# Optimization experiments

Hardware: AMD Instinct MI355X
Metric: run time of the kernel (lower is better)

Reference implementation:

```python
import jax, jax.numpy as jnp
import numpy as np

B, N, C, T = 16, 96, 4, 256
H, DT, DP, P, TOUT = 128, 16, 128, 4, 64
DIN = H + DT
LEAK = 0.1


def setup_inputs():
    key = jax.random.key(0)
    ks = jax.random.split(key, 16)
    rn = lambda k, shp, s: jax.random.normal(k, shp, dtype=jnp.float32) * s
    return {
        'X_in': jax.random.normal(ks[0], (B, N, C, T), dtype=jnp.float32),
        'phases': jax.random.randint(ks[1], (B,), 0, P),
        'gru_Wih': rn(ks[2], (N, 3 * H, C), 0.1),
        'gru_Whh': rn(ks[3], (N, 3 * H, H), 0.08),
        'gru_bih': jnp.zeros((N, 3 * H), jnp.float32),
        'gru_bhh': jnp.zeros((N, 3 * H), jnp.float32),
        'ln_g': jnp.ones((H,), jnp.float32),
        'ln_b': jnp.zeros((H,), jnp.float32),
        'tpos_w': rn(ks[4], (DT, 1), 0.5),
        'tpos_b': jnp.zeros((DT,), jnp.float32),
        'S': rn(ks[5], (P, N, N), 0.1),
        'G': rn(ks[6], (P, N), 0.1),
        'W_self': rn(ks[7], (DP, DIN), 0.05),
        'W_neigh': rn(ks[8], (DP, DIN), 0.05),
        'sn_u': jax.random.normal(ks[9], (DP,), dtype=jnp.float32),
        'k_w': rn(ks[10], (DP, DP), 0.05),
        'v_w': rn(ks[11], (DP, DP), 0.05),
        'cell_Wih': rn(ks[12], (3 * DP, DP + C), 0.05),
        'cell_Whh': rn(ks[13], (3 * DP, DP), 0.05),
        'cell_bih': jnp.zeros((3 * DP,), jnp.float32),
        'cell_bhh': jnp.zeros((3 * DP,), jnp.float32),
        'read_w': rn(ks[14], (C, DP), 0.05),
        'read_b': jnp.zeros((C,), jnp.float32),
        'log_tau': jnp.asarray(np.log(1.0 / np.sqrt(DP)), dtype=jnp.float32),
    }


def _encode(X, Wih, Whh, bih, bhh, g, b):
    # Per-region GRU (distinct weights per node), torch gate order r,z,n.
    xs = jnp.moveaxis(X, -1, 0)  # [T,B,N,C]
    h0 = jnp.zeros((B, N, H), X.dtype)
    def step(h, xt):
        gi = jnp.einsum('bnc,ngc->bng', xt, Wih) + bih
        gh = jnp.einsum('bnh,ngh->bng', h, Whh) + bhh
        ir, iz, inn = jnp.split(gi, 3, axis=-1)
        hr, hz, hn = jnp.split(gh, 3, axis=-1)
        r = jax.nn.sigmoid(ir + hr)
        z = jax.nn.sigmoid(iz + hz)
        n = jnp.tanh(inn + r * hn)
        hnew = (1.0 - z) * n + z * h
        return hnew, hnew
    _, ys = jax.lax.scan(step, h0, xs)  # [T,B,N,H]
    mu = ys.mean(-1, keepdims=True)
    var = ys.var(-1, keepdims=True)
    ys = (ys - mu) * jax.lax.rsqrt(var + 1e-5) * g + b
    return jnp.moveaxis(ys, 0, 2)  # [B,N,T,H]


def _phase_adj(S, G, phases):
    I = jnp.eye(N, dtype=S.dtype)
    S0 = S * (1.0 - I)
    denom = jnp.clip(jnp.abs(S0).sum(-1, keepdims=True), 1e-6, None)
    An = S0 / denom
    gg = jax.nn.softplus(G) + 1e-6
    gg = gg * (N / jnp.clip(gg.sum(-1, keepdims=True), 1e-6, None))
    return An[phases] * gg[phases][..., None]  # [B,N,N]


def _spectral_normalize(W, u):
    v = W.T @ u
    v = v / (jnp.linalg.norm(v) + 1e-12)
    u2 = W @ v
    u2 = u2 / (jnp.linalg.norm(u2) + 1e-12)
    u2 = jax.lax.stop_gradient(u2)
    v = jax.lax.stop_gradient(v)
    sigma = u2 @ (W @ v)
    return W / sigma


def _head(Z, A, k_w, v_w, cWih, cWhh, cbih, cbhh, rw, rb, log_tau):
    BN = B * N
    M = Z.reshape(BN, T, DP)
    K = M @ k_w.T
    V = M @ v_w.T
    h0 = M[:, -1, :]
    y0 = jnp.zeros((BN, C), Z.dtype)
    scale = jnp.exp(log_tau)
    def step(carry, _):
        h, y = carry
        yb = y.reshape(B, N, C)
        yb = yb + 0.3 * jnp.einsum('bij,bjc->bic', A, yb)
        y = yb.reshape(BN, C)
        scores = jnp.einsum('mtd,md->mt', K, h) * scale
        alpha = jax.nn.softmax(scores, axis=-1)
        ctx = jnp.einsum('mt,mtd->md', alpha, V)
        inp = jnp.concatenate([ctx, y], axis=-1)
        gi = inp @ cWih.T + cbih
        gh = h @ cWhh.T + cbhh
        ir, iz, inn = jnp.split(gi, 3, axis=-1)
        hr, hz, hn = jnp.split(gh, 3, axis=-1)
        r = jax.nn.sigmoid(ir + hr)
        z = jax.nn.sigmoid(iz + hz)
        n = jnp.tanh(inn + r * hn)
        h = (1.0 - z) * n + z * h
        y_t = h @ rw.T + rb + y
        return (h, y_t), y_t
    _, ys = jax.lax.scan(step, (h0, y0), None, length=TOUT)  # [TOUT,BN,C]
    return jnp.transpose(ys, (1, 2, 0)).reshape(B, N, C, TOUT)


def _forward(X_in, phases, gru_Wih, gru_Whh, gru_bih, gru_bhh, ln_g, ln_b,
             tpos_w, tpos_b, S, G, W_self, W_neigh, sn_u, k_w, v_w,
             cell_Wih, cell_Whh, cell_bih, cell_bhh, read_w, read_b, log_tau):
    Henc = _encode(X_in, gru_Wih, gru_Whh, gru_bih, gru_bhh, ln_g, ln_b)  # [B,N,T,H]
    t = jnp.linspace(0.0, 1.0, T).astype(jnp.float32).reshape(T, 1)
    u = jnp.tanh(t @ tpos_w.T + tpos_b)  # [T,DT]
    u = jnp.broadcast_to(u[None, None], (B, N, T, DT))
    Hc = jnp.concatenate([Henc, u], axis=-1)  # [B,N,T,DIN]
    A = _phase_adj(S, G, phases)
    Wsn = _spectral_normalize(W_neigh, sn_u)
    Hs = Hc @ W_self.T
    Hn = Hc @ Wsn.T
    Zn = jnp.einsum('bij,bjtd->bitd', A, Hn)
    Zpre = Hs + Zn
    Z = jnp.where(Zpre >= 0, Zpre, LEAK * Zpre)
    Y_delta = _head(Z, A, k_w, v_w, cell_Wih, cell_Whh, cell_bih, cell_bhh,
                    read_w, read_b, log_tau)
    x_last = X_in[..., -1]  # [B,N,C]
    Y_hat = x_last[..., None] + Y_delta
    return Y_hat, Y_hat[..., 0:1]


def reference(X_in, phases, gru_Wih, gru_Whh, gru_bih, gru_bhh, ln_g, ln_b,
              tpos_w, tpos_b, S, G, W_self, W_neigh, sn_u, k_w, v_w,
              cell_Wih, cell_Whh, cell_bih, cell_bhh, read_w, read_b, log_tau):
    return _forward(X_in, phases, gru_Wih, gru_Whh, gru_bih, gru_bhh, ln_g, ln_b,
                    tpos_w, tpos_b, S, G, W_self, W_neigh, sn_u, k_w, v_w,
                    cell_Wih, cell_Whh, cell_bih, cell_bhh, read_w, read_b, log_tau)
```

## Files before the change

kernel.cpp:

```cpp
#include <hip/hip_runtime.h>
#include <stdint.h>

typedef unsigned int u32;
typedef unsigned short u16;
typedef __attribute__((ext_vector_type(8))) short s8v;
typedef __attribute__((ext_vector_type(8))) __bf16 bf16x8;
typedef __attribute__((ext_vector_type(4))) float f32x4;

#define OFF_HENC 0ull
#define OFF_M    100663296ull
#define OFF_APF  201326592ull
#define OFF_APB  201474048ull
#define OFF_WNF  201547776ull
#define OFF_WSF  201588736ull
#define OFF_KWF  201629696ull
#define OFF_VWF  201662464ull
#define OFF_WIHF 201695232ull
#define OFF_WHHF 201793536ull
#define OFF_CWY  201891840ull
#define OFF_UPAD 201897984ull
#define OFF_SCAL 201914368ull
#define OFF_HH   201914624ull
#define OFF_Y    202701056ull

__device__ __forceinline__ u16 f2bf(float f) {
  u32 u = __float_as_uint(f);
  u32 r = u + 0x7fffu + ((u >> 16) & 1u);
  return (u16)(r >> 16);
}
__device__ __forceinline__ float bf2f(u16 h) { return __uint_as_float(((u32)h) << 16); }
__device__ __forceinline__ float blo(u32 u) { return __uint_as_float(u << 16); }
__device__ __forceinline__ float bhi(u32 u) { return __uint_as_float(u & 0xffff0000u); }
__device__ __forceinline__ float sigm(float x) { return 1.f / (1.f + __expf(-x)); }
__device__ __forceinline__ float tanh_f(float x) {
  float a = fminf(fabsf(x), 15.f);
  float e = __expf(2.f * a);
  float t = (e - 1.f) / (e + 1.f);
  return copysignf(t, x);
}
__device__ __forceinline__ f32x4 MFMA(s8v a, s8v b, f32x4 c) {
  return __builtin_amdgcn_mfma_f32_16x16x32_bf16(
      __builtin_bit_cast(bf16x8, a), __builtin_bit_cast(bf16x8, b), c, 0, 0, 0);
}

__global__ void k0a(const float* __restrict__ S, const float* __restrict__ G,
                    const float* __restrict__ Wn, const float* __restrict__ snu,
                    const float* __restrict__ logtau, const float* __restrict__ tpw,
                    const float* __restrict__ tpb, const float* __restrict__ cWih,
                    float* __restrict__ Apf, u16* __restrict__ Apb,
                    float* __restrict__ scal, u16* __restrict__ upad,
                    float* __restrict__ cWy) {
  int tid = threadIdx.x;
  int blk = blockIdx.x;
  if (blk < 4) {
    int p = blk;
    __shared__ float gg[96];
    __shared__ float gfac;
    if (tid < 96) {
      float x = G[p * 96 + tid];
      float sp = fmaxf(x, 0.f) + log1pf(__expf(-fabsf(x)));
      gg[tid] = sp + 1e-6f;
    }
    __syncthreads();
    if (tid == 0) {
      float s = 0;
      for (int i = 0; i < 96; ++i) s += gg[i];
      gfac = 96.f / fmaxf(s, 1e-6f);
    }
    __syncthreads();
    if (tid < 96) {
      int i = tid;
      const float* srow = S + ((size_t)p * 96 + i) * 96;
      float den = 0;
      for (int j = 0; j < 96; ++j) { float v = (j == i) ? 0.f : srow[j]; den += fabsf(v); }
      den = fmaxf(den, 1e-6f);
      float sc = gg[i] * gfac / den;
      for (int j = 0; j < 96; ++j) {
        float v = (j == i) ? 0.f : srow[j];
        float a = v * sc;
        Apf[((size_t)p * 96 + i) * 96 + j] = a;
        Apb[((size_t)p * 96 + i) * 96 + j] = f2bf(a);
      }
    }
  } else if (blk == 4) {
    __shared__ float sv[144];
    __shared__ float su[128];
    __shared__ float snorm;
    if (tid < 144) {
      float a = 0;
      for (int d = 0; d < 128; ++d) a += Wn[d * 144 + tid] * snu[d];
      sv[tid] = a;
    }
    __syncthreads();
    if (tid == 0) {
      float s = 0;
      for (int j = 0; j < 144; ++j) s += sv[j] * sv[j];
      snorm = sqrtf(s) + 1e-12f;
    }
    __syncthreads();
    if (tid < 144) sv[tid] = sv[tid] / snorm;
    __syncthreads();
    if (tid < 128) {
      float a = 0;
      for (int j = 0; j < 144; ++j) a += Wn[tid * 144 + j] * sv[j];
      su[tid] = a;
    }
    __syncthreads();
    if (tid == 0) {
      float ss = 0;
      for (int d = 0; d < 128; ++d) ss += su[d] * su[d];
      float nu = sqrtf(ss);
      float sigma = ss / (nu + 1e-12f);
      scal[0] = 1.f / sigma;
      scal[1] = __expf(logtau[0]);
    }
  } else {
    for (int idx = tid; idx < 256 * 32; idx += 256) {
      int t = idx >> 5, kk = idx & 31;
      float v = 0.f;
      if (kk < 16) v = tanh_f((float)t * (1.f / 255.f) * tpw[kk] + tpb[kk]);
      upad[idx] = f2bf(v);
    }
    for (int idx = tid; idx < 1536; idx += 256)
      cWy[idx] = cWih[(idx >> 2) * 132 + 128 + (idx & 3)];
  }
}
// ... 144 lines not shown
  const int b = blockIdx.x >> 8, t = blockIdx.x & 255;
  const int p = phases[b];
  const int lane = threadIdx.x & 63, w = threadIdx.x >> 6;
  const int colt = lane & 15, grp = lane >> 4;
  __shared__ __align__(16) u16 Hc[96][168];
  __shared__ __align__(16) u16 HnT[128][104];
  __shared__ float lnG[128], lnB[128];

  const u16* src = Henc + ((size_t)b * 96 * 256 + t) * 128;
  for (int u = threadIdx.x; u < 96 * 16; u += 256) {
    int j = u >> 4, ch = u & 15;
    *(uint4*)&Hc[j][ch * 8] = *(const uint4*)(src + (size_t)j * 256 * 128 + ch * 8);
  }
  for (int u = threadIdx.x; u < 96 * 16; u += 256) {
    int j = u >> 4, ch = u & 15;
    *(u32*)&Hc[j][128 + ch * 2] = *(const u32*)(upad + t * 32 + ch * 2);
  }
  if (threadIdx.x < 128) {
    lnG[threadIdx.x] = lng[threadIdx.x];
    lnB[threadIdx.x] = lnb[threadIdx.x];
  }
  __syncthreads();
  if (threadIdx.x < 96) {
    int j = threadIdx.x;
    float s = 0.f, q = 0.f;
#pragma unroll 4
    for (int d = 0; d < 128; ++d) {
      float v = bf2f(Hc[j][d]);
      s += v; q += v * v;
    }
    float mu = s * (1.f / 128.f);
    float var = q * (1.f / 128.f) - mu * mu;
    float rs = rsqrtf(var + 1e-5f);
#pragma unroll 4
    for (int d = 0; d < 128; ++d) {
      float v = bf2f(Hc[j][d]);
      Hc[j][d] = f2bf((v - mu) * rs * lnG[d] + lnB[d]);
    }
  }
  __syncthreads();
  for (int jj = 0; jj < 12; ++jj) {
    int job = w * 12 + jj;
    int jt = job >> 3, ct = job & 7;
    f32x4 acc = {0.f, 0.f, 0.f, 0.f};
#pragma unroll
    for (int kq = 0; kq < 5; ++kq) {
      s8v a = *(const s8v*)(const void*)&Hc[jt * 16 + colt][kq * 32 + grp * 8];
      acc = MFMA(a, WnF[(ct * 5 + kq) * 64 + lane], acc);
    }
    int d = ct * 16 + colt, j0 = jt * 16 + grp * 4;
    u32 w0 = ((u32)f2bf(acc[1]) << 16) | f2bf(acc[0]);
    u32 w1 = ((u32)f2bf(acc[3]) << 16) | f2bf(acc[2]);
    *(u32*)&HnT[d][j0] = w0;
    *(u32*)&HnT[d][j0 + 2] = w1;
  }
  __syncthreads();
  for (int jj = 0; jj < 12; ++jj) {
    int job = w * 12 + jj;
    int it = job >> 3, ct = job & 7;
    f32x4 accZ = {0.f, 0.f, 0.f, 0.f}, accS = accZ;
#pragma unroll
    for (int kq = 0; kq < 3; ++kq) {
      s8v a = *(const s8v*)(const void*)(Apb + ((size_t)p * 96 + it * 16 + colt) * 96 + kq * 32 + grp * 8);
      s8v bb = *(const s8v*)(const void*)&HnT[ct * 16 + colt][kq * 32 + grp * 8];
      accZ = MFMA(a, bb, accZ);
    }
#pragma unroll
    for (int kq = 0; kq < 5; ++kq) {
      s8v a = *(const s8v*)(const void*)&Hc[it * 16 + colt][kq * 32 + grp * 8];
      accS = MFMA(a, WsF[(ct * 5 + kq) * 64 + lane], accS);
    }
    int d = ct * 16 + colt;
#pragma unroll
    for (int r = 0; r < 4; ++r) {
      int i = it * 16 + grp * 4 + r;
      float z = accS[r] + accZ[r];
      z = z >= 0.f ? z : 0.1f * z;
      M[(((size_t)b * 96 + i) * 256 + t) * 128 + d] = f2bf(z);
      if (t == 255) hh[((size_t)b * 96 + i) * 128 + d] = z;
    }
  }
}

__launch_bounds__(512)
__global__ void k4_step(int k, const u16* __restrict__ M, float* __restrict__ hh,
                        const float* __restrict__ yin, float* __restrict__ yout,
                        const float* __restrict__ Apf, const int* __restrict__ phases,
                        const float* __restrict__ scal,
                        const s8v* __restrict__ kwF, const s8v* __restrict__ vwF,
                        const s8v* __restrict__ wiF, const s8v* __restrict__ whF,
                        const float* __restrict__ cWy, const float* __restrict__ cbih,
                        const float* __restrict__ cbhh, const float* __restrict__ rw,
                        const float* __restrict__ rb, const float* __restrict__ X,
                        float* __restrict__ out) {
  const int bl = blockIdx.x;
  const int b = bl >> 4, n0 = (bl & 15) * 6, m0 = b * 96 + n0;
  const int lane = threadIdx.x & 63, w = threadIdx.x >> 6;
  const int colt = lane & 15, grp = lane >> 4;
  __shared__ float hfl[6][128];
  __shared__ __align__(16) u16 hb[16][136];
  __shared__ __align__(16) u16 qb[6][128];
  __shared__ __align__(16) u16 sb[16][136];
  __shared__ __align__(16) u16 cxb[16][136];
  __shared__ __align__(16) float macc[6][16][128];
  __shared__ float mmd[6][16][2];
  __shared__ float gi_l[6][392];
  __shared__ float gh_l[6][392];
  __shared__ float ypl[6][4];
  const float scale = scal[1];

  for (int idx = threadIdx.x; idx < 2048; idx += 512) {
    int i = idx >> 7, d = idx & 127;
    float hv = 0.f;
    if (i < 6) {
      hv = hh[(size_t)(m0 + i) * 128 + d];
      hfl[i][d] = hv;
    } else {
      sb[i][d] = 0;
      cxb[i][d] = 0;
    }
    hb[i][d] = f2bf(hv);
  }
  if (w < 6) {
    int i = w, ni = n0 + w;
    const float* arow = Apf + ((size_t)phases[b] * 96 + ni) * 96;
    float acc[4] = {0.f, 0.f, 0.f, 0.f};
    for (int j = lane; j < 96; j += 64) {
      float av = arow[j];
      const float* yr = yin + ((size_t)b * 96 + j) * 4;
      acc[0] += av * yr[0]; acc[1] += av * yr[1];
      acc[2] += av * yr[2]; acc[3] += av * yr[3];
    }
#pragma unroll
    for (int mm = 1; mm < 64; mm <<= 1) {
#pragma unroll
      for (int c = 0; c < 4; ++c) acc[c] += __shfl_xor(acc[c], mm);
    }
    if (lane < 4) ypl[i][lane] = yin[((size_t)b * 96 + ni) * 4 + lane] + 0.3f * acc[lane];
  }
  __syncthreads();

  {
    int ct = w;
    f32x4 acc = {0.f, 0.f, 0.f, 0.f};
#pragma unroll
    for (int kq = 0; kq < 4; ++kq) {
      s8v a = *(const s8v*)(const void*)&hb[colt][kq * 32 + grp * 8];
      acc = MFMA(a, kwF[(ct * 4 + kq) * 64 + lane], acc);
    }
#pragma unroll
    for (int r = 0; r < 4; ++r) {
      int i = grp * 4 + r;
      if (i < 6) qb[i][ct * 16 + colt] = f2bf(acc[r] * scale);
    }
  }
  __syncthreads();

#pragma unroll 1
  for (int uu = 0; uu < 3; ++uu) {
    int u = w + uu * 8;
    int mi = u >> 2, qq = u & 3;
    float qf[8];
    const u32* qsrc = (const u32*)&qb[mi][colt * 8];
#pragma unroll
    for (int x = 0; x < 4; ++x) { u32 v = qsrc[x]; qf[2 * x] = blo(v); qf[2 * x + 1] = bhi(v); }
    const u16* mp = M + ((size_t)(m0 + mi) * 256 + qq * 64 + grp) * 128 + colt * 8;
    uint4 mv[16];
#pragma unroll
    for (int it = 0; it < 16; ++it) mv[it] = *(const uint4*)(mp + it * 512);
    float p[16];
#pragma unroll
    for (int it = 0; it < 16; ++it) {
      uint4 v = mv[it];
      float pp = blo(v.x) * qf[0] + bhi(v.x) * qf[1] + blo(v.y) * qf[2] + bhi(v.y) * qf[3]
               + blo(v.z) * qf[4] + bhi(v.z) * qf[5] + blo(v.w) * qf[6] + bhi(v.w) * qf[7];
      pp += __shfl_xor(pp, 1); pp += __shfl_xor(pp, 2);
      pp += __shfl_xor(pp, 4); pp += __shfl_xor(pp, 8);
      p[it] = pp;
    }
    float mx = p[0];
#pragma unroll
    for (int it = 1; it < 16; ++it) mx = fmaxf(mx, p[it]);
    float den = 0.f;
    float acc[8] = {0.f, 0.f, 0.f, 0.f, 0.f, 0.f, 0.f, 0.f};
#pragma unroll
    for (int it = 0; it < 16; ++it) {
      float wgt = __expf(p[it] - mx);
      den += wgt;
      uint4 v = mv[it];
      acc[0] += wgt * blo(v.x); acc[1] += wgt * bhi(v.x);
      acc[2] += wgt * blo(v.y); acc[3] += wgt * bhi(v.y);
      acc[4] += wgt * blo(v.z); acc[5] += wgt * bhi(v.z);
      acc[6] += wgt * blo(v.w); acc[7] += wgt * bhi(v.w);
    }
    int su = qq * 4 + grp;
    float* dst = &macc[mi][su][colt * 8];
#pragma unroll
    for (int j = 0; j < 8; ++j) dst[j] = acc[j];
    if (colt == 0) { mmd[mi][su][0] = mx; mmd[mi][su][1] = den; }
  }
  __syncthreads();

  if (w < 6) {
    int i = w;
    float MX = -3.0e38f;
#pragma unroll
    for (int uy = 0; uy < 16; ++uy) MX = fmaxf(MX, mmd[i][uy][0]);
    float DEN = 0.f, s0 = 0.f, s1 = 0.f;
    int c0 = lane * 2;
#pragma unroll
    for (int uy = 0; uy < 16; ++uy) {
      float fac = __expf(mmd[i][uy][0] - MX);
      DEN += fac * mmd[i][uy][1];
      s0 += fac * macc[i][uy][c0];
      s1 += fac * macc[i][uy][c0 + 1];
    }
    float rden = 1.f / DEN;
    *(u32*)&sb[i][c0] = ((u32)f2bf(s1 * rden) << 16) | f2bf(s0 * rden);
  }
  __syncthreads();

  {
    int ct = w;
    f32x4 acc = {0.f, 0.f, 0.f, 0.f};
#pragma unroll
    for (int kq = 0; kq < 4; ++kq) {
      s8v a = *(const s8v*)(const void*)&sb[colt][kq * 32 + grp * 8];
      acc = MFMA(a, vwF[(ct * 4 + kq) * 64 + lane], acc);
    }
#pragma unroll
    for (int r = 0; r < 4; ++r) {
      int i = grp * 4 + r;
      if (i < 6) cxb[i][ct * 16 + colt] = f2bf(acc[r]);
    }
  }
  __syncthreads();

  for (int jj = 0; jj < 6; ++jj) {
    int job = w * 6 + jj;
    int gsel = (job >= 24) ? 1 : 0;
    int ct = job - gsel * 24;
    const u16(*asrc)[136] = gsel ? hb : cxb;
    const s8v* wf = gsel ? whF : wiF;
    f32x4 acc = {0.f, 0.f, 0.f, 0.f};
#pragma unroll
    for (int kq = 0; kq < 4; ++kq) {
      s8v a = *(const s8v*)(const void*)&asrc[colt][kq * 32 + grp * 8];
      acc = MFMA(a, wf[(ct * 4 + kq) * 64 + lane], acc);
    }
    float* dst = gsel ? &gh_l[0][0] : &gi_l[0][0];
#pragma unroll
    for (int r = 0; r < 4; ++r) {
      int i = grp * 4 + r;
      if (i < 6) dst[i * 392 + ct * 16 + colt] = acc[r];
    }
  }
  __syncthreads();

  if (w < 6) {
    int i = w, m = m0 + i;
    float yp0 = ypl[i][0], yp1 = ypl[i][1], yp2 = ypl[i][2], yp3 = ypl[i][3];
    float hn2[2];
#pragma unroll
    for (int q = 0; q < 2; ++q) {
      int d = lane + q * 64;
      float gir = gi_l[i][d] + cbih[d];
      float giz = gi_l[i][d + 128] + cbih[d + 128];
      float gin = gi_l[i][d + 256] + cbih[d + 256];
      const float* wy0 = cWy + (size_t)d * 4;
      const float* wy1 = cWy + (size_t)(d + 128) * 4;
      const float* wy2 = cWy + (size_t)(d + 256) * 4;
      gir += yp0 * wy0[0] + yp1 * wy0[1] + yp2 * wy0[2] + yp3 * wy0[3];
      giz += yp0 * wy1[0] + yp1 * wy1[1] + yp2 * wy1[2] + yp3 * wy1[3];
      gin += yp0 * wy2[0] + yp1 * wy2[1] + yp2 * wy2[2] + yp3 * wy2[3];
      float ghr = gh_l[i][d] + cbhh[d];
      float ghz = gh_l[i][d + 128] + cbhh[d + 128];
      float ghn = gh_l[i][d + 256] + cbhh[d + 256];
      float rr = sigm(gir + ghr);
      float zz = sigm(giz + ghz);
      float nn = tanh_f(gin + rr * ghn);
      float hv = (1.f - zz) * nn + zz * hfl[i][d];
      hh[(size_t)m * 128 + d] = hv;
      hn2[q] = hv;
    }
    float p0 = hn2[0] * rw[0 * 128 + lane] + hn2[1] * rw[0 * 128 + lane + 64];
    float p1 = hn2[0] * rw[1 * 128 + lane] + hn2[1] * rw[1 * 128 + lane + 64];
    float p2 = hn2[0] * rw[2 * 128 + lane] + hn2[1] * rw[2 * 128 + lane + 64];
    float p3 = hn2[0] * rw[3 * 128 + lane] + hn2[1] * rw[3 * 128 + lane + 64];
#pragma unroll
    for (int mm = 1; mm < 64; mm <<= 1) {
      p0 += __shfl_xor(p0, mm); p1 += __shfl_xor(p1, mm);
      p2 += __shfl_xor(p2, mm); p3 += __shfl_xor(p3, mm);
    }
    if (lane < 4) {
      int c = lane;
      float pv = (c == 0) ? p0 : (c == 1) ? p1 : (c == 2) ? p2 : p3;
      float ypc = (c == 0) ? yp0 : (c == 1) ? yp1 : (c == 2) ? yp2 : yp3;
      float yv = pv + rb[c] + ypc;
      yout[(size_t)m * 4 + c] = yv;
      float xl = X[((size_t)m * 4 + c) * 256 + 255];
      float Yh = xl + yv;
      out[((size_t)m * 4 + c) * 64 + k] = Yh;
      if (k == 0) out[393216 + (size_t)m * 4 + c] = Yh;
    }
  }
}

extern "C" void kernel_launch(void* const* d_in, const int* in_sizes, int n_in,
                              void* d_out, int out_size, void* d_ws, size_t ws_size,
                              hipStream_t stream) {
  const float* X      = (const float*)d_in[0];
  const int*   phases = (const int*)d_in[1];
  const float* Wih    = (const float*)d_in[2];
  const float* Whh    = (const float*)d_in[3];
  const float* bih    = (const float*)d_in[4];
  const float* bhh    = (const float*)d_in[5];
  const float* lng    = (const float*)d_in[6];
  const float* lnb    = (const float*)d_in[7];
  const float* tpw    = (const float*)d_in[8];
  const float* tpb    = (const float*)d_in[9];
  const float* S      = (const float*)d_in[10];
  const float* G      = (const float*)d_in[11];
  const float* Wself  = (const float*)d_in[12];
  const float* Wneigh = (const float*)d_in[13];
  const float* snu    = (const float*)d_in[14];
  const float* kw     = (const float*)d_in[15];
  const float* vw     = (const float*)d_in[16];
  const float* cWih   = (const float*)d_in[17];
  const float* cWhh   = (const float*)d_in[18];
  const float* cbih   = (const float*)d_in[19];
  const float* cbhh   = (const float*)d_in[20];
  const float* rw     = (const float*)d_in[21];
  const float* rb     = (const float*)d_in[22];
  const float* ltau   = (const float*)d_in[23];

  char* ws = (char*)d_ws;
  u16*   Henc = (u16*)(ws + OFF_HENC);
  u16*   Mb   = (u16*)(ws + OFF_M);
  float* Apf  = (float*)(ws + OFF_APF);
  u16*   Apb  = (u16*)(ws + OFF_APB);
  u16*   WnF  = (u16*)(ws + OFF_WNF);
  u16*   WsF  = (u16*)(ws + OFF_WSF);
  u16*   kwF  = (u16*)(ws + OFF_KWF);
  u16*   vwF  = (u16*)(ws + OFF_VWF);
  u16*   wiF  = (u16*)(ws + OFF_WIHF);
  u16*   whF  = (u16*)(ws + OFF_WHHF);
  float* cWy  = (float*)(ws + OFF_CWY);
  u16*   upad = (u16*)(ws + OFF_UPAD);
  float* scal = (float*)(ws + OFF_SCAL);
  float* hh   = (float*)(ws + OFF_HH);

  hipMemsetAsync(ws + OFF_Y, 0, 49152, stream);
  hipLaunchKernelGGL(k0a, dim3(6), dim3(256), 0, stream,
                     S, G, Wneigh, snu, ltau, tpw, tpb, cWih, Apf, Apb, scal, upad, cWy);
  hipLaunchKernelGGL(k0b, dim3(672), dim3(256), 0, stream,
                     Wneigh, Wself, kw, vw, cWih, cWhh, scal, WnF, WsF, kwF, vwF, wiF, whF);
  hipLaunchKernelGGL(k1_encode, dim3(96), dim3(512), 0, stream,
                     X, Wih, Whh, bih, bhh, Henc);
  hipLaunchKernelGGL(k3_mix, dim3(4096), dim3(256), 0, stream,
                     Henc, upad, Apb, phases, lng, lnb,
                     (const s8v*)WnF, (const s8v*)WsF, Mb, hh);
  for (int k = 0; k < 64; ++k) {
    const float* yi = (const float*)(ws + OFF_Y + (size_t)(k & 1) * 24576);
    float*       yo = (float*)(ws + OFF_Y + (size_t)((k + 1) & 1) * 24576);
    hipLaunchKernelGGL(k4_step, dim3(256), dim3(512), 0, stream,
                       k, Mb, hh, yi, yo, Apf, phases, scal,
                       (const s8v*)kwF, (const s8v*)vwF, (const s8v*)wiF, (const s8v*)whF,
                       cWy, cbih, cbhh, rw, rb, X, (float*)d_out);
  }
}
```

Before: 2.158 ms.

## Fuse decode steps into persistent kernel with register-resident memory and group barriers

Replaces the 64 per-step launches of the decoder with one persistent kernel that loops over steps. Each block keeps its slice of the attention memory M in registers for all steps and carries the hidden state in shared memory. A per-batch atomic barrier synchronises the 16 blocks that share the y vector. It also uses bf16 dot2 for scores and stages small weights in LDS. The aim is to remove repeated global reads of M and launch overhead, at the cost of very high register pressure and a reliance on all blocks being co-resident.

Measured after the change: 7.835 ms. 263% more time.

```diff
diff --git a/kernel.cpp b/kernel.cpp
--- a/kernel.cpp
+++ b/kernel.cpp
@@ -5,6 +5,7 @@
 typedef unsigned short u16;
 typedef __attribute__((ext_vector_type(8))) short s8v;
 typedef __attribute__((ext_vector_type(8))) __bf16 bf16x8;
+typedef __attribute__((ext_vector_type(2))) __bf16 bf16x2;
 typedef __attribute__((ext_vector_type(4))) float f32x4;
 
 #define OFF_HENC 0ull
@@ -22,6 +23,7 @@
 #define OFF_SCAL 201914368ull
 #define OFF_HH   201914624ull
 #define OFF_Y    202701056ull
+#define OFF_BAR  202750208ull
 
 __device__ __forceinline__ u16 f2bf(float f) {
   u32 u = __float_as_uint(f);
@@ -42,6 +44,16 @@
   return __builtin_amdgcn_mfma_f32_16x16x32_bf16(
       __builtin_bit_cast(bf16x8, a), __builtin_bit_cast(bf16x8, b), c, 0, 0, 0);
 }
+
+#if __has_builtin(__builtin_amdgcn_fdot2_f32_bf16)
+#define HAS_DOT2 1
+__device__ __forceinline__ float dot2bf(u32 a, u32 b, float c) {
+  return __builtin_amdgcn_fdot2_f32_bf16(__builtin_bit_cast(bf16x2, a),
+                                         __builtin_bit_cast(bf16x2, b), c, false);
+}
+#else
+#define HAS_DOT2 0
+#endif
 
 __global__ void k0a(const float* __restrict__ S, const float* __restrict__ G,
                     const float* __restrict__ Wn, const float* __restrict__ snu,
@@ -352,34 +364,70 @@
   }
 }
 
-__launch_bounds__(512)
-__global__ void k4_step(int k, const u16* __restrict__ M, float* __restrict__ hh,
-                        const float* __restrict__ yin, float* __restrict__ yout,
-                        const float* __restrict__ Apf, const int* __restrict__ phases,
-                        const float* __restrict__ scal,
-                        const s8v* __restrict__ kwF, const s8v* __restrict__ vwF,
-                        const s8v* __restrict__ wiF, const s8v* __restrict__ whF,
-                        const float* __restrict__ cWy, const float* __restrict__ cbih,
-                        const float* __restrict__ cbhh, const float* __restrict__ rw,
-                        const float* __restrict__ rb, const float* __restrict__ X,
-                        float* __restrict__ out) {
+__device__ __forceinline__ void group_barrier(int* cnt, int* gen) {
+  __syncthreads();
+  if (threadIdx.x == 0) {
+    int g = __hip_atomic_load(gen, __ATOMIC_RELAXED, __HIP_MEMORY_SCOPE_AGENT);
+    int v = __hip_atomic_fetch_add(cnt, 1, __ATOMIC_ACQ_REL, __HIP_MEMORY_SCOPE_AGENT);
+    if (v == 15) {
+      __hip_atomic_store(cnt, 0, __ATOMIC_RELAXED, __HIP_MEMORY_SCOPE_AGENT);
+      __hip_atomic_fetch_add(gen, 1, __ATOMIC_ACQ_REL, __HIP_MEMORY_SCOPE_AGENT);
+    } else {
+      while (__hip_atomic_load(gen, __ATOMIC_ACQUIRE, __HIP_MEMORY_SCOPE_AGENT) == g)
+        __builtin_amdgcn_s_sleep(1);
+    }
+  }
+  __syncthreads();
+}
+
+__launch_bounds__(256, 1)
+__global__ void k4p(const u16* __restrict__ M, const float* __restrict__ hh,
+                    float* __restrict__ ybuf, int* __restrict__ bar,
+                    const float* __restrict__ Apf, const int* __restrict__ phases,
+                    const float* __restrict__ scal,
+                    const s8v* __restrict__ kwF, const s8v* __restrict__ vwF,
+                    const s8v* __restrict__ wiF, const s8v* __restrict__ whF,
+                    const float* __restrict__ cWy, const float* __restrict__ cbih,
+                    const float* __restrict__ cbhh, const float* __restrict__ rw,
+                    const float* __restrict__ rb, const float* __restrict__ X,
+                    float* __restrict__ out) {
   const int bl = blockIdx.x;
   const int b = bl >> 4, n0 = (bl & 15) * 6, m0 = b * 96 + n0;
   const int lane = threadIdx.x & 63, w = threadIdx.x >> 6;
   const int colt = lane & 15, grp = lane >> 4;
+  int* cnt = bar + b;
+  int* gen = bar + 16 + b;
+
   __shared__ float hfl[6][128];
   __shared__ __align__(16) u16 hb[16][136];
   __shared__ __align__(16) u16 qb[6][128];
   __shared__ __align__(16) u16 sb[16][136];
   __shared__ __align__(16) u16 cxb[16][136];
-  __shared__ __align__(16) float macc[6][16][128];
-  __shared__ float mmd[6][16][2];
+  __shared__ __align__(16) float macc[6][4][128];
+  __shared__ float mmd[6][4][2];
   __shared__ float gi_l[6][392];
   __shared__ float gh_l[6][392];
   __shared__ float ypl[6][4];
+  __shared__ float Arows[6][96];
+  __shared__ float cbl_i[384], cbl_h[384];
+  __shared__ float cWyl[384][4];
+  __shared__ float rwl[4][128];
+  __shared__ float rbl[4];
+  __shared__ float xlast[6][4];
+
+  const int p = phases[b];
   const float scale = scal[1];
 
-  for (int idx = threadIdx.x; idx < 2048; idx += 512) {
+  uint4 Mreg[6][16];
+#pragma unroll
+  for (int mi = 0; mi < 6; ++mi) {
+    const u16* base = M + (((size_t)(m0 + mi) * 256) + w * 64 + grp) * 128 + colt * 8;
+#pragma unroll
+    for (int it = 0; it < 16; ++it)
+      Mreg[mi][it] = *(const uint4*)(base + (size_t)it * 512);
+  }
+
+  for (int idx = threadIdx.x; idx < 2048; idx += 256) {
     int i = idx >> 7, d = idx & 127;
     float hv = 0.f;
     if (i < 6) {
@@ -391,188 +439,249 @@
     }
     hb[i][d] = f2bf(hv);
   }
-  if (w < 6) {
-    int i = w, ni = n0 + w;
-    const float* arow = Apf + ((size_t)phases[b] * 96 + ni) * 96;
-    float acc[4] = {0.f, 0.f, 0.f, 0.f};
-    for (int j = lane; j < 96; j += 64) {
-      float av = arow[j];
-      const float* yr = yin + ((size_t)b * 96 + j) * 4;
-      acc[0] += av * yr[0]; acc[1] += av * yr[1];
-      acc[2] += av * yr[2]; acc[3] += av * yr[3];
-    }
-#pragma unroll
-    for (int mm = 1; mm < 64; mm <<= 1) {
-#pragma unroll
-      for (int c = 0; c < 4; ++c) acc[c] += __shfl_xor(acc[c], mm);
-    }
-    if (lane < 4) ypl[i][lane] = yin[((size_t)b * 96 + ni) * 4 + lane] + 0.3f * acc[lane];
-  }
+  for (int idx = threadIdx.x; idx < 576; idx += 256) {
+    int i = idx / 96, j = idx % 96;
+    Arows[i][j] = Apf[((size_t)p * 96 + (n0 + i)) * 96 + j];
+  }
+  for (int idx = threadIdx.x; idx < 384; idx += 256) {
+    cbl_i[idx] = cbih[idx];
+    cbl_h[idx] = cbhh[idx];
+  }
+  for (int idx = threadIdx.x; idx < 1536; idx += 256)
+    (&cWyl[0][0])[idx] = cWy[idx];
+  for (int idx = threadIdx.x; idx < 512; idx += 256)
+    (&rwl[0][0])[idx] = rw[idx];
+  if (threadIdx.x < 4) rbl[threadIdx.x] = rb[threadIdx.x];
+  if (threadIdx.x < 24)
+    xlast[threadIdx.x >> 2][threadIdx.x & 3] =
+        X[((size_t)(m0 + (threadIdx.x >> 2)) * 4 + (threadIdx.x & 3)) * 256 + 255];
   __syncthreads();
 
-  {
-    int ct = w;
-    f32x4 acc = {0.f, 0.f, 0.f, 0.f};
-#pragma unroll
-    for (int kq = 0; kq < 4; ++kq) {
-      s8v a = *(const s8v*)(const void*)&hb[colt][kq * 32 + grp * 8];
-      acc = MFMA(a, kwF[(ct * 4 + kq) * 64 + lane], acc);
-    }
-#pragma unroll
-    for (int r = 0; r < 4; ++r) {
-      int i = grp * 4 + r;
-      if (i < 6) qb[i][ct * 16 + colt] = f2bf(acc[r] * scale);
-    }
-  }
-  __syncthreads();
-
 #pragma unroll 1
-  for (int uu = 0; uu < 3; ++uu) {
-    int u = w + uu * 8;
-    int mi = u >> 2, qq = u & 3;
-    float qf[8];
-    const u32* qsrc = (const u32*)&qb[mi][colt * 8];
-#pragma unroll
-    for (int x = 0; x < 4; ++x) { u32 v = qsrc[x]; qf[2 * x] = blo(v); qf[2 * x + 1] = bhi(v); }
-    const u16* mp = M + ((size_t)(m0 + mi) * 256 + qq * 64 + grp) * 128 + colt * 8;
-    uint4 mv[16];
-#pragma unroll
-    for (int it = 0; it < 16; ++it) mv[it] = *(const uint4*)(mp + it * 512);
-    float p[16];
-#pragma unroll
-    for (int it = 0; it < 16; ++it) {
-      uint4 v = mv[it];
-      float pp = blo(v.x) * qf[0] + bhi(v.x) * qf[1] + blo(v.y) * qf[2] + bhi(v.y) * qf[3]
-               + blo(v.z) * qf[4] + bhi(v.z) * qf[5] + blo(v.w) * qf[6] + bhi(v.w) * qf[7];
-      pp += __shfl_xor(pp, 1); pp += __shfl_xor(pp, 2);
-      pp += __shfl_xor(pp, 4); pp += __shfl_xor(pp, 8);
-      p[it] = pp;
-    }
-    float mx = p[0];
-#pragma unroll
-    for (int it = 1; it < 16; ++it) mx = fmaxf(mx, p[it]);
-    float den = 0.f;
-    float acc[8] = {0.f, 0.f, 0.f, 0.f, 0.f, 0.f, 0.f, 0.f};
-#pragma unroll
-    for (int it = 0; it < 16; ++it) {
-      float wgt = __expf(p[it] - mx);
-      den += wgt;
-      uint4 v = mv[it];
-      acc[0] += wgt * blo(v.x); acc[1] += wgt * bhi(v.x);
-      acc[2] += wgt * blo(v.y); acc[3] += wgt * bhi(v.y);
-      acc[4] += wgt * blo(v.z); acc[5] += wgt * bhi(v.z);
-      acc[6] += wgt * blo(v.w); acc[7] += wgt * bhi(v.w);
-    }
-    int su = qq * 4 + grp;
-    float* dst = &macc[mi][su][colt * 8];
-#pragma unroll
-    for (int j = 0; j < 8; ++j) dst[j] = acc[j];
-    if (colt == 0) { mmd[mi][su][0] = mx; mmd[mi][su][1] = den; }
-  }
-  __syncthreads();
-
-  if (w < 6) {
-    int i = w;
-    float MX = -3.0e38f;
-#pragma unroll
-    for (int uy = 0; uy < 16; ++uy) MX = fmaxf(MX, mmd[i][uy][0]);
-    float DEN = 0.f, s0 = 0.f, s1 = 0.f;
-    int c0 = lane * 2;
-#pragma unroll
-    for (int uy = 0; uy < 16; ++uy) {
-      float fac = __expf(mmd[i][uy][0] - MX);
-      DEN += fac * mmd[i][uy][1];
-      s0 += fac * macc[i][uy][c0];
-      s1 += fac * macc[i][uy][c0 + 1];
-    }
-    float rden = 1.f / DEN;
-    *(u32*)&sb[i][c0] = ((u32)f2bf(s1 * rden) << 16) | f2bf(s0 * rden);
-  }
-  __syncthreads();
-
-  {
-    int ct = w;
-    f32x4 acc = {0.f, 0.f, 0.f, 0.f};
-#pragma unroll
-    for (int kq = 0; kq < 4; ++kq) {
-      s8v a = *(const s8v*)(const void*)&sb[colt][kq * 32 + grp * 8];
-      acc = MFMA(a, vwF[(ct * 4 + kq) * 64 + lane], acc);
-    }
-#pragma unroll
-    for (int r = 0; r < 4; ++r) {
-      int i = grp * 4 + r;
-      if (i < 6) cxb[i][ct * 16 + colt] = f2bf(acc[r]);
-    }
-  }
-  __syncthreads();
-
-  for (int jj = 0; jj < 6; ++jj) {
-    int job = w * 6 + jj;
-    int gsel = (job >= 24) ? 1 : 0;
-    int ct = job - gsel * 24;
-    const u16(*asrc)[136] = gsel ? hb : cxb;
-    const s8v* wf = gsel ? whF : wiF;
-    f32x4 acc = {0.f, 0.f, 0.f, 0.f};
-#pragma unroll
-    for (int kq = 0; kq < 4; ++kq) {
-      s8v a = *(const s8v*)(const void*)&asrc[colt][kq * 32 + grp * 8];
-      acc = MFMA(a, wf[(ct * 4 + kq) * 64 + lane], acc);
-    }
-    float* dst = gsel ? &gh_l[0][0] : &gi_l[0][0];
-#pragma unroll
-    for (int r = 0; r < 4; ++r) {
-      int i = grp * 4 + r;
-      if (i < 6) dst[i * 392 + ct * 16 + colt] = acc[r];
-    }
-  }
-  __syncthreads();
-
-  if (w < 6) {
-    int i = w, m = m0 + i;
-    float yp0 = ypl[i][0], yp1 = ypl[i][1], yp2 = ypl[i][2], yp3 = ypl[i][3];
-    float hn2[2];
-#pragma unroll
-    for (int q = 0; q < 2; ++q) {
-      int d = lane + q * 64;
-      float gir = gi_l[i][d] + cbih[d];
-      float giz = gi_l[i][d + 128] + cbih[d + 128];
-      float gin = gi_l[i][d + 256] + cbih[d + 256];
-      const float* wy0 = cWy + (size_t)d * 4;
-      const float* wy1 = cWy + (size_t)(d + 128) * 4;
-      const float* wy2 = cWy + (size_t)(d + 256) * 4;
-      gir += yp0 * wy0[0] + yp1 * wy0[1] + yp2 * wy0[2] + yp3 * wy0[3];
-      giz += yp0 * wy1[0] + yp1 * wy1[1] + yp2 * wy1[2] + yp3 * wy1[3];
-      gin += yp0 * wy2[0] + yp1 * wy2[1] + yp2 * wy2[2] + yp3 * wy2[3];
-      float ghr = gh_l[i][d] + cbhh[d];
-      float ghz = gh_l[i][d + 128] + cbhh[d + 128];
-      float ghn = gh_l[i][d + 256] + cbhh[d + 256];
-      float rr = sigm(gir + ghr);
-      float zz = sigm(giz + ghz);
-      float nn = tanh_f(gin + rr * ghn);
-      float hv = (1.f - zz) * nn + zz * hfl[i][d];
-      hh[(size_t)m * 128 + d] = hv;
-      hn2[q] = hv;
-    }
-    float p0 = hn2[0] * rw[0 * 128 + lane] + hn2[1] * rw[0 * 128 + lane + 64];
-    float p1 = hn2[0] * rw[1 * 128 + lane] + hn2[1] * rw[1 * 128 + lane + 64];
-    float p2 = hn2[0] * rw[2 * 128 + lane] + hn2[1] * rw[2 * 128 + lane + 64];
-    float p3 = hn2[0] * rw[3 * 128 + lane] + hn2[1] * rw[3 * 128 + lane + 64];
-#pragma unroll
-    for (int mm = 1; mm < 64; mm <<= 1) {
-      p0 += __shfl_xor(p0, mm); p1 += __shfl_xor(p1, mm);
-      p2 += __shfl_xor(p2, mm); p3 += __shfl_xor(p3, mm);
-    }
-    if (lane < 4) {
-      int c = lane;
-      float pv = (c == 0) ? p0 : (c == 1) ? p1 : (c == 2) ? p2 : p3;
-      float ypc = (c == 0) ? yp0 : (c == 1) ? yp1 : (c == 2) ? yp2 : yp3;
-      float yv = pv + rb[c] + ypc;
-      yout[(size_t)m * 4 + c] = yv;
-      float xl = X[((size_t)m * 4 + c) * 256 + 255];
-      float Yh = xl + yv;
-      out[((size_t)m * 4 + c) * 64 + k] = Yh;
-      if (k == 0) out[393216 + (size_t)m * 4 + c] = Yh;
-    }
+  for (int k = 0; k < 64; ++k) {
+    const float* yin = ybuf + (size_t)(k & 1) * 6144;
+    float* yout = ybuf + (size_t)((k + 1) & 1) * 6144;
+
+#pragma unroll 1
+    for (int rr = 0; rr < 2; ++rr) {
+      if (rr == 0 || w < 2) {
+        int mi = (rr == 0) ? w : 4 + w;
+        int ni = n0 + mi;
+        float a0 = 0.f, a1 = 0.f, a2 = 0.f, a3 = 0.f;
+#pragma unroll 1
+        for (int j = lane; j < 96; j += 64) {
+          float av = Arows[mi][j];
+          float* yr = (float*)(yin + ((size_t)b * 96 + j) * 4);
+          a0 += av * __hip_atomic_load(yr + 0, __ATOMIC_RELAXED, __HIP_MEMORY_SCOPE_AGENT);
+          a1 += av * __hip_atomic_load(yr + 1, __ATOMIC_RELAXED, __HIP_MEMORY_SCOPE_AGENT);
+          a2 += av * __hip_atomic_load(yr + 2, __ATOMIC_RELAXED, __HIP_MEMORY_SCOPE_AGENT);
+          a3 += av * __hip_atomic_load(yr + 3, __ATOMIC_RELAXED, __HIP_MEMORY_SCOPE_AGENT);
+        }
+#pragma unroll
+        for (int mm = 1; mm < 64; mm <<= 1) {
+          a0 += __shfl_xor(a0, mm); a1 += __shfl_xor(a1, mm);
+          a2 += __shfl_xor(a2, mm); a3 += __shfl_xor(a3, mm);
+        }
+        if (lane < 4) {
+          float av = (lane == 0) ? a0 : (lane == 1) ? a1 : (lane == 2) ? a2 : a3;
+          float yo = __hip_atomic_load((float*)(yin + ((size_t)b * 96 + ni) * 4 + lane),
+                                       __ATOMIC_RELAXED, __HIP_MEMORY_SCOPE_AGENT);
+          ypl[mi][lane] = yo + 0.3f * av;
+        }
+      }
+    }
+
+#pragma unroll
+    for (int cc = 0; cc < 2; ++cc) {
+      int ct = w * 2 + cc;
+      f32x4 acc = {0.f, 0.f, 0.f, 0.f};
+#pragma unroll
+      for (int kq = 0; kq < 4; ++kq) {
+        s8v a = *(const s8v*)(const void*)&hb[colt][kq * 32 + grp * 8];
+        acc = MFMA(a, kwF[(ct * 4 + kq) * 64 + lane], acc);
+      }
+#pragma unroll
+      for (int r = 0; r < 4; ++r) {
+        int i = grp * 4 + r;
+        if (i < 6) qb[i][ct * 16 + colt] = f2bf(acc[r] * scale);
+      }
+    }
+    __syncthreads();
+
+#pragma unroll
+    for (int mi = 0; mi < 6; ++mi) {
+      u32 qw[4];
+      float qf[8];
+      {
+        const u32* qsrc = (const u32*)&qb[mi][colt * 8];
+#pragma unroll
+        for (int x = 0; x < 4; ++x) {
+          qw[x] = qsrc[x];
+          qf[2 * x] = blo(qw[x]); qf[2 * x + 1] = bhi(qw[x]);
+        }
+      }
+      float pv[16];
+#pragma unroll
+      for (int it = 0; it < 16; ++it) {
+        uint4 v = Mreg[mi][it];
+#if HAS_DOT2
+        float pp = dot2bf(v.x, qw[0], dot2bf(v.y, qw[1], dot2bf(v.z, qw[2], dot2bf(v.w, qw[3], 0.f))));
+#else
+        float pp = blo(v.x) * qf[0] + bhi(v.x) * qf[1] + blo(v.y) * qf[2] + bhi(v.y) * qf[3]
+                 + blo(v.z) * qf[4] + bhi(v.z) * qf[5] + blo(v.w) * qf[6] + bhi(v.w) * qf[7];
+#endif
+        pp += __shfl_xor(pp, 1); pp += __shfl_xor(pp, 2);
+        pp += __shfl_xor(pp, 4); pp += __shfl_xor(pp, 8);
+        pv[it] = pp;
+      }
+      float mx = pv[0];
+#pragma unroll
+      for (int it = 1; it < 16; ++it) mx = fmaxf(mx, pv[it]);
+      mx = fmaxf(mx, __shfl_xor(mx, 16));
+      mx = fmaxf(mx, __shfl_xor(mx, 32));
+      float den = 0.f;
+      float acc[8] = {0.f, 0.f, 0.f, 0.f, 0.f, 0.f, 0.f, 0.f};
+#pragma unroll
+      for (int it = 0; it < 16; ++it) {
+        float wgt = __expf(pv[it] - mx);
+        den += wgt;
+        uint4 v = Mreg[mi][it];
+        acc[0] += wgt * blo(v.x); acc[1] += wgt * bhi(v.x);
+        acc[2] += wgt * blo(v.y); acc[3] += wgt * bhi(v.y);
+        acc[4] += wgt * blo(v.z); acc[5] += wgt * bhi(v.z);
+        acc[6] += wgt * blo(v.w); acc[7] += wgt * bhi(v.w);
+      }
+#pragma unroll
+      for (int j = 0; j < 8; ++j) {
+        acc[j] += __shfl_xor(acc[j], 16);
+        acc[j] += __shfl_xor(acc[j], 32);
+      }
+      den += __shfl_xor(den, 16);
+      den += __shfl_xor(den, 32);
+      if (grp == 0) {
+        float* dst = &macc[mi][w][colt * 8];
+#pragma unroll
+        for (int j = 0; j < 8; ++j) dst[j] = acc[j];
+        if (colt == 0) { mmd[mi][w][0] = mx; mmd[mi][w][1] = den; }
+      }
+    }
+    __syncthreads();
+
+#pragma unroll
+    for (int r2 = 0; r2 < 2; ++r2) {
+      int item = threadIdx.x + r2 * 256;
+      if (item < 384) {
+        int mi = item >> 6;
+        int c0 = (item & 63) * 2;
+        float MX = fmaxf(fmaxf(mmd[mi][0][0], mmd[mi][1][0]),
+                         fmaxf(mmd[mi][2][0], mmd[mi][3][0]));
+        float DEN = 0.f, s0 = 0.f, s1 = 0.f;
+#pragma unroll
+        for (int wv = 0; wv < 4; ++wv) {
+          float fac = __expf(mmd[mi][wv][0] - MX);
+          DEN += fac * mmd[mi][wv][1];
+          s0 += fac * macc[mi][wv][c0];
+          s1 += fac * macc[mi][wv][c0 + 1];
+        }
+        float rden = 1.f / DEN;
+        *(u32*)&sb[mi][c0] = ((u32)f2bf(s1 * rden) << 16) | f2bf(s0 * rden);
+      }
+    }
+    __syncthreads();
+
+#pragma unroll
+    for (int cc = 0; cc < 2; ++cc) {
+      int ct = w * 2 + cc;
+      f32x4 acc = {0.f, 0.f, 0.f, 0.f};
+#pragma unroll
+      for (int kq = 0; kq < 4; ++kq) {
+        s8v a = *(const s8v*)(const void*)&sb[colt][kq * 32 + grp * 8];
+        acc = MFMA(a, vwF[(ct * 4 + kq) * 64 + lane], acc);
+      }
+#pragma unroll
+      for (int r = 0; r < 4; ++r) {
+        int i = grp * 4 + r;
+        if (i < 6) cxb[i][ct * 16 + colt] = f2bf(acc[r]);
+      }
+    }
+    __syncthreads();
+
+#pragma unroll 1
+    for (int jj = 0; jj < 12; ++jj) {
+      int job = w * 12 + jj;
+      int gsel = (job >= 24) ? 1 : 0;
+      int ct = job - gsel * 24;
+      const u16(*asrc)[136] = gsel ? hb : cxb;
+      const s8v* wf = gsel ? whF : wiF;
+      f32x4 acc = {0.f, 0.f, 0.f, 0.f};
+#pragma unroll
+      for (int kq = 0; kq < 4; ++kq) {
+        s8v a = *(const s8v*)(const void*)&asrc[colt][kq * 32 + grp * 8];
+        acc = MFMA(a, wf[(ct * 4 + kq) * 64 + lane], acc);
+      }
+      float* dst = gsel ? &gh_l[0][0] : &gi_l[0][0];
+#pragma unroll
+      for (int r = 0; r < 4; ++r) {
+        int i = grp * 4 + r;
+        if (i < 6) dst[i * 392 + ct * 16 + colt] = acc[r];
+      }
+    }
+    __syncthreads();
+
+#pragma unroll 1
+    for (int rr = 0; rr < 2; ++rr) {
+      if (rr == 0 || w < 2) {
+        int mi = (rr == 0) ? w : 4 + w;
+        int m = m0 + mi;
+        float yp0 = ypl[mi][0], yp1 = ypl[mi][1], yp2 = ypl[mi][2], yp3 = ypl[mi][3];
+        float hn2[2];
+#pragma unroll
+        for (int q = 0; q < 2; ++q) {
+          int d = lane + q * 64;
+          float gir = gi_l[mi][d] + cbl_i[d];
+          float giz = gi_l[mi][d + 128] + cbl_i[d + 128];
+          float gin = gi_l[mi][d + 256] + cbl_i[d + 256];
+          const float* wy0 = &cWyl[d][0];
+          const float* wy1 = &cWyl[d + 128][0];
+          const float* wy2 = &cWyl[d + 256][0];
+          gir += yp0 * wy0[0] + yp1 * wy0[1] + yp2 * wy0[2] + yp3 * wy0[3];
+          giz += yp0 * wy1[0] + yp1 * wy1[1] + yp2 * wy1[2] + yp3 * wy1[3];
+          gin += yp0 * wy2[0] + yp1 * wy2[1] + yp2 * wy2[2] + yp3 * wy2[3];
+          float ghr = gh_l[mi][d] + cbl_h[d];
+          float ghz = gh_l[mi][d + 128] + cbl_h[d + 128];
+          float ghn = gh_l[mi][d + 256] + cbl_h[d + 256];
+          float rg = sigm(gir + ghr);
+          float zz = sigm(giz + ghz);
+          float nn = tanh_f(gin + rg * ghn);
+          float hv = (1.f - zz) * nn + zz * hfl[mi][d];
+          hfl[mi][d] = hv;
+          hb[mi][d] = f2bf(hv);
+          hn2[q] = hv;
+        }
+        float p0 = hn2[0] * rwl[0][lane] + hn2[1] * rwl[0][(lane + 64) & 127];
+        float p1 = hn2[0] * rwl[1][lane] + hn2[1] * rwl[1][(lane + 64) & 127];
+        float p2 = hn2[0] * rwl[2][lane] + hn2[1] * rwl[2][(lane + 64) & 127];
+        float p3 = hn2[0] * rwl[3][lane] + hn2[1] * rwl[3][(lane + 64) & 127];
+#pragma unroll
+        for (int mm = 1; mm < 64; mm <<= 1) {
+          p0 += __shfl_xor(p0, mm); p1 += __shfl_xor(p1, mm);
+          p2 += __shfl_xor(p2, mm); p3 += __shfl_xor(p3, mm);
+        }
+        if (lane < 4) {
+          int c = lane;
+          float pvv = (c == 0) ? p0 : (c == 1) ? p1 : (c == 2) ? p2 : p3;
+          float ypc = (c == 0) ? yp0 : (c == 1) ? yp1 : (c == 2) ? yp2 : yp3;
+          float yv = pvv + rbl[c] + ypc;
+          __hip_atomic_store((float*)(yout + (size_t)m * 4 + c), yv,
+                             __ATOMIC_RELAXED, __HIP_MEMORY_SCOPE_AGENT);
+          float Yh = xlast[mi][c] + yv;
+          out[((size_t)m * 4 + c) * 64 + k] = Yh;
+          if (k == 0) out[393216 + (size_t)m * 4 + c] = Yh;
+        }
+      }
+    }
+
+    if (k < 63) group_barrier(cnt, gen);
   }
 }
 
@@ -619,8 +728,10 @@
   u16*   upad = (u16*)(ws + OFF_UPAD);
   float* scal = (float*)(ws + OFF_SCAL);
   float* hh   = (float*)(ws + OFF_HH);
-
-  hipMemsetAsync(ws + OFF_Y, 0, 49152, stream);
+  float* ybuf = (float*)(ws + OFF_Y);
+  int*   bar  = (int*)(ws + OFF_BAR);
+
+  hipMemsetAsync(ws + OFF_Y, 0, 49152 + 128, stream);
   hipLaunchKernelGGL(k0a, dim3(6), dim3(256), 0, stream,
                      S, G, Wneigh, snu, ltau, tpw, tpb, cWih, Apf, Apb, scal, upad, cWy);
   hipLaunchKernelGGL(k0b, dim3(672), dim3(256), 0, stream,
@@ -630,12 +741,8 @@
   hipLaunchKernelGGL(k3_mix, dim3(4096), dim3(256), 0, stream,
                      Henc, upad, Apb, phases, lng, lnb,
                      (const s8v*)WnF, (const s8v*)WsF, Mb, hh);
-  for (int k = 0; k < 64; ++k) {
-    const float* yi = (const float*)(ws + OFF_Y + (size_t)(k & 1) * 24576);
-    float*       yo = (float*)(ws + OFF_Y + (size_t)((k + 1) & 1) * 24576);
-    hipLaunchKernelGGL(k4_step, dim3(256), dim3(512), 0, stream,
-                       k, Mb, hh, yi, yo, Apf, phases, scal,
-                       (const s8v*)kwF, (const s8v*)vwF, (const s8v*)wiF, (const s8v*)whF,
-                       cWy, cbih, cbhh, rw, rb, X, (float*)d_out);
-  }
-}
+  hipLaunchKernelGGL(k4p, dim3(256), dim3(256), 0, stream,
+                     Mb, hh, ybuf, bar, Apf, phases, scal,
+                     (const s8v*)kwF, (const s8v*)vwF, (const s8v*)wiF, (const s8v*)whF,
+                     cWy, cbih, cbhh, rw, rb, X, (float*)d_out);
+}
```

## Quantize attention memory M to int8 with per-row scales for decode steps

Applied to the files above, without the earlier changes.

Adds a kernel that converts the bf16 memory tensor M into unsigned int8 with a per-(node,time) scale and a 128 offset. The 64 decode-step kernels then read the int8 copy, apply the offset correction in algebraic form to both scores and the weighted sums, and rescale. This halves the bytes streamed from M on every step, which is repeated 64 times. The cost is one extra quantization pass over M and lower precision in the attention keys and values, which could push results past the tolerance.

New measurement: 2.077 ms. 1.04x faster.

```diff
diff --git a/kernel.cpp b/kernel.cpp
--- a/kernel.cpp
+++ b/kernel.cpp
@@ -3,25 +3,28 @@
 
 typedef unsigned int u32;
 typedef unsigned short u16;
+typedef unsigned char u8;
 typedef __attribute__((ext_vector_type(8))) short s8v;
 typedef __attribute__((ext_vector_type(8))) __bf16 bf16x8;
 typedef __attribute__((ext_vector_type(4))) float f32x4;
 
 #define OFF_HENC 0ull
 #define OFF_M    100663296ull
-#define OFF_APF  201326592ull
-#define OFF_APB  201474048ull
-#define OFF_WNF  201547776ull
-#define OFF_WSF  201588736ull
-#define OFF_KWF  201629696ull
-#define OFF_VWF  201662464ull
-#define OFF_WIHF 201695232ull
-#define OFF_WHHF 201793536ull
-#define OFF_CWY  201891840ull
-#define OFF_UPAD 201897984ull
-#define OFF_SCAL 201914368ull
-#define OFF_HH   201914624ull
-#define OFF_Y    202701056ull
+#define OFF_MI8  201326592ull
+#define OFF_MSCL 251658240ull
+#define OFF_APF  253231104ull
+#define OFF_APB  253378560ull
+#define OFF_WNF  253452288ull
+#define OFF_WSF  253493248ull
+#define OFF_KWF  253534208ull
+#define OFF_VWF  253566976ull
+#define OFF_WIHF 253599744ull
+#define OFF_WHHF 253698048ull
+#define OFF_CWY  253796352ull
+#define OFF_UPAD 253802496ull
+#define OFF_SCAL 253818880ull
+#define OFF_HH   253819136ull
+#define OFF_Y    254605568ull
 
 __device__ __forceinline__ u16 f2bf(float f) {
   u32 u = __float_as_uint(f);
@@ -42,6 +45,10 @@
   return __builtin_amdgcn_mfma_f32_16x16x32_bf16(
       __builtin_bit_cast(bf16x8, a), __builtin_bit_cast(bf16x8, b), c, 0, 0, 0);
 }
+__device__ __forceinline__ float ub0(u32 x) { return (float)(x & 0xffu); }
+__device__ __forceinline__ float ub1(u32 x) { return (float)((x >> 8) & 0xffu); }
+__device__ __forceinline__ float ub2(u32 x) { return (float)((x >> 16) & 0xffu); }
+__device__ __forceinline__ float ub3(u32 x) { return (float)((x >> 24) & 0xffu); }
 
 __global__ void k0a(const float* __restrict__ S, const float* __restrict__ G,
                     const float* __restrict__ Wn, const float* __restrict__ snu,
@@ -352,8 +359,39 @@
   }
 }
 
+__launch_bounds__(256)
+__global__ void k3b(const u16* __restrict__ Mbf, u8* __restrict__ Mi8,
+                    float* __restrict__ Mscl) {
+  const size_t m = blockIdx.x;
+  const int t = threadIdx.x;
+  const u16* src = Mbf + (m * 256 + t) * 128;
+  float vals[128];
+  float mx = 0.f;
+#pragma unroll 8
+  for (int d = 0; d < 128; ++d) {
+    float f = bf2f(src[d]);
+    vals[d] = f;
+    mx = fmaxf(mx, fabsf(f));
+  }
+  float scale = mx * (1.f / 127.f);
+  float inv = (mx > 0.f) ? (127.f / mx) : 0.f;
+  u32* dst = (u32*)(Mi8 + (m * 256 + t) * 128);
+#pragma unroll 8
+  for (int dw = 0; dw < 32; ++dw) {
+    u32 packed = 0;
+#pragma unroll
+    for (int j = 0; j < 4; ++j) {
+      int q = (int)rintf(vals[dw * 4 + j] * inv) + 128;
+      packed |= ((u32)(q & 0xff)) << (8 * j);
+    }
+    dst[dw] = packed;
+  }
+  Mscl[m * 256 + t] = scale;
+}
+
 __launch_bounds__(512)
-__global__ void k4_step(int k, const u16* __restrict__ M, float* __restrict__ hh,
+__global__ void k4_step(int k, const u8* __restrict__ Mi8, const float* __restrict__ Mscl,
+                        float* __restrict__ hh,
                         const float* __restrict__ yin, float* __restrict__ yout,
                         const float* __restrict__ Apf, const int* __restrict__ phases,
                         const float* __restrict__ scal,
@@ -373,7 +411,8 @@
   __shared__ __align__(16) u16 sb[16][136];
   __shared__ __align__(16) u16 cxb[16][136];
   __shared__ __align__(16) float macc[6][16][128];
-  __shared__ float mmd[6][16][2];
+  __shared__ float mmd[6][16][4];
+  __shared__ float sclL[6][256];
   __shared__ float gi_l[6][392];
   __shared__ float gh_l[6][392];
   __shared__ float ypl[6][4];
@@ -391,6 +430,10 @@
     }
     hb[i][d] = f2bf(hv);
   }
+  for (int idx = threadIdx.x; idx < 1536; idx += 512) {
+    int mi = idx >> 8, t = idx & 255;
+    sclL[mi][t] = Mscl[(size_t)(m0 + mi) * 256 + t];
+  }
   if (w < 6) {
     int i = w, ni = n0 + w;
     const float* arow = Apf + ((size_t)phases[b] * 96 + ni) * 96;
@@ -434,40 +477,48 @@
     const u32* qsrc = (const u32*)&qb[mi][colt * 8];
 #pragma unroll
     for (int x = 0; x < 4; ++x) { u32 v = qsrc[x]; qf[2 * x] = blo(v); qf[2 * x + 1] = bhi(v); }
-    const u16* mp = M + ((size_t)(m0 + mi) * 256 + qq * 64 + grp) * 128 + colt * 8;
-    uint4 mv[16];
-#pragma unroll
-    for (int it = 0; it < 16; ++it) mv[it] = *(const uint4*)(mp + it * 512);
+    float qs = qf[0] + qf[1] + qf[2] + qf[3] + qf[4] + qf[5] + qf[6] + qf[7];
+    qs += __shfl_xor(qs, 1); qs += __shfl_xor(qs, 2);
+    qs += __shfl_xor(qs, 4); qs += __shfl_xor(qs, 8);
+    const u8* mp = Mi8 + ((size_t)(m0 + mi) * 256 + qq * 64 + grp) * 128 + colt * 8;
+    uint2 mv[16];
+#pragma unroll
+    for (int it = 0; it < 16; ++it) mv[it] = *(const uint2*)(mp + (size_t)it * 512);
+    float scl[16];
+#pragma unroll
+    for (int it = 0; it < 16; ++it) scl[it] = sclL[mi][qq * 64 + it * 4 + grp];
     float p[16];
 #pragma unroll
     for (int it = 0; it < 16; ++it) {
-      uint4 v = mv[it];
-      float pp = blo(v.x) * qf[0] + bhi(v.x) * qf[1] + blo(v.y) * qf[2] + bhi(v.y) * qf[3]
-               + blo(v.z) * qf[4] + bhi(v.z) * qf[5] + blo(v.w) * qf[6] + bhi(v.w) * qf[7];
+      uint2 v = mv[it];
+      float pp = qf[0] * ub0(v.x) + qf[1] * ub1(v.x) + qf[2] * ub2(v.x) + qf[3] * ub3(v.x)
+               + qf[4] * ub0(v.y) + qf[5] * ub1(v.y) + qf[6] * ub2(v.y) + qf[7] * ub3(v.y);
       pp += __shfl_xor(pp, 1); pp += __shfl_xor(pp, 2);
       pp += __shfl_xor(pp, 4); pp += __shfl_xor(pp, 8);
-      p[it] = pp;
+      p[it] = scl[it] * (pp - 128.f * qs);
     }
     float mx = p[0];
 #pragma unroll
     for (int it = 1; it < 16; ++it) mx = fmaxf(mx, p[it]);
-    float den = 0.f;
+    float den = 0.f, gs = 0.f;
     float acc[8] = {0.f, 0.f, 0.f, 0.f, 0.f, 0.f, 0.f, 0.f};
 #pragma unroll
     for (int it = 0; it < 16; ++it) {
       float wgt = __expf(p[it] - mx);
       den += wgt;
-      uint4 v = mv[it];
-      acc[0] += wgt * blo(v.x); acc[1] += wgt * bhi(v.x);
-      acc[2] += wgt * blo(v.y); acc[3] += wgt * bhi(v.y);
-      acc[4] += wgt * blo(v.z); acc[5] += wgt * bhi(v.z);
-      acc[6] += wgt * blo(v.w); acc[7] += wgt * bhi(v.w);
+      float g = wgt * scl[it];
+      gs += g;
+      uint2 v = mv[it];
+      acc[0] += g * ub0(v.x); acc[1] += g * ub1(v.x);
+      acc[2] += g * ub2(v.x); acc[3] += g * ub3(v.x);
+      acc[4] += g * ub0(v.y); acc[5] += g * ub1(v.y);
+      acc[6] += g * ub2(v.y); acc[7] += g * ub3(v.y);
     }
     int su = qq * 4 + grp;
     float* dst = &macc[mi][su][colt * 8];
 #pragma unroll
     for (int j = 0; j < 8; ++j) dst[j] = acc[j];
-    if (colt == 0) { mmd[mi][su][0] = mx; mmd[mi][su][1] = den; }
+    if (colt == 0) { mmd[mi][su][0] = mx; mmd[mi][su][1] = den; mmd[mi][su][2] = gs; }
   }
   __syncthreads();
 
@@ -476,17 +527,19 @@
     float MX = -3.0e38f;
 #pragma unroll
     for (int uy = 0; uy < 16; ++uy) MX = fmaxf(MX, mmd[i][uy][0]);
-    float DEN = 0.f, s0 = 0.f, s1 = 0.f;
+    float DEN = 0.f, GS = 0.f, s0 = 0.f, s1 = 0.f;
     int c0 = lane * 2;
 #pragma unroll
     for (int uy = 0; uy < 16; ++uy) {
       float fac = __expf(mmd[i][uy][0] - MX);
       DEN += fac * mmd[i][uy][1];
+      GS += fac * mmd[i][uy][2];
       s0 += fac * macc[i][uy][c0];
       s1 += fac * macc[i][uy][c0 + 1];
     }
     float rden = 1.f / DEN;
-    *(u32*)&sb[i][c0] = ((u32)f2bf(s1 * rden) << 16) | f2bf(s0 * rden);
+    float corr = 128.f * GS;
+    *(u32*)&sb[i][c0] = ((u32)f2bf((s1 - corr) * rden) << 16) | f2bf((s0 - corr) * rden);
   }
   __syncthreads();
 
@@ -607,6 +660,8 @@
   char* ws = (char*)d_ws;
   u16*   Henc = (u16*)(ws + OFF_HENC);
   u16*   Mb   = (u16*)(ws + OFF_M);
+  u8*    Mi8  = (u8*)(ws + OFF_MI8);
+  float* Mscl = (float*)(ws + OFF_MSCL);
   float* Apf  = (float*)(ws + OFF_APF);
   u16*   Apb  = (u16*)(ws + OFF_APB);
   u16*   WnF  = (u16*)(ws + OFF_WNF);
@@ -630,11 +685,12 @@
   hipLaunchKernelGGL(k3_mix, dim3(4096), dim3(256), 0, stream,
                      Henc, upad, Apb, phases, lng, lnb,
                      (const s8v*)WnF, (const s8v*)WsF, Mb, hh);
+  hipLaunchKernelGGL(k3b, dim3(1536), dim3(256), 0, stream, Mb, Mi8, Mscl);
   for (int k = 0; k < 64; ++k) {
     const float* yi = (const float*)(ws + OFF_Y + (size_t)(k & 1) * 24576);
     float*       yo = (float*)(ws + OFF_Y + (size_t)((k + 1) & 1) * 24576);
     hipLaunchKernelGGL(k4_step, dim3(256), dim3(512), 0, stream,
-                       k, Mb, hh, yi, yo, Apf, phases, scal,
+                       k, Mi8, Mscl, hh, yi, yo, Apf, phases, scal,
                        (const s8v*)kwF, (const s8v*)vwF, (const s8v*)wiF, (const s8v*)whF,
                        cWy, cbih, cbhh, rw, rb, X, (float*)d_out);
   }
```
